# Optimization experiments

Hardware: AMD Instinct MI355X
Metric: run time of the kernel (lower is better)

## Reference

```python
import jax, jax.numpy as jnp
import numpy as np

N = 10000      # nodes
E = 160000     # edges
G = 128        # graphs in batch
DIMS = [16, 32, 32]  # in_channels, then conv output dims
HID = 25       # edge-MLP hidden width
EPS = 1e-5     # batch-norm eps


def setup_inputs() -> dict:
    key = jax.random.key(0)
    ks = iter(jax.random.split(key, 40))
    inp = {}
    inp["x"] = jax.random.normal(next(ks), (N, DIMS[0]), dtype=jnp.float32)
    inp["edge_attr"] = jax.random.uniform(next(ks), (E, 3), dtype=jnp.float32)
    inp["edge_index"] = jax.random.randint(next(ks), (2, E), 0, N, dtype=jnp.int32)
    inp["batch"] = jnp.sort(jax.random.randint(next(ks), (N,), 0, G, dtype=jnp.int32))
    for i in range(2):
        din, dout = DIMS[i], DIMS[i + 1]
        inp[f"w1_{i}"] = jax.random.normal(next(ks), (3, HID), dtype=jnp.float32) * 0.3
        inp[f"b1_{i}"] = jnp.zeros((HID,), jnp.float32)
        inp[f"g_{i}"] = jnp.ones((HID,), jnp.float32)
        inp[f"be_{i}"] = jnp.zeros((HID,), jnp.float32)
        inp[f"w2_{i}"] = jax.random.normal(next(ks), (HID, din * dout), dtype=jnp.float32) * 0.05
        inp[f"b2_{i}"] = jnp.zeros((din * dout,), jnp.float32)
        inp[f"wr_{i}"] = jax.random.normal(next(ks), (din, dout), dtype=jnp.float32) * 0.1
        inp[f"bc_{i}"] = jnp.zeros((dout,), jnp.float32)
    inp["wfc"] = jax.random.normal(next(ks), (DIMS[-1], 1), dtype=jnp.float32) * 0.1
    inp["bfc"] = jnp.zeros((1,), jnp.float32)
    return inp


def _ecn(x, edge_attr, layers, wfc, bfc, edge_index, batch):
    src, dst = edge_index[0], edge_index[1]
    deg = jax.ops.segment_sum(jnp.ones((E,), x.dtype), dst, num_segments=N)
    deg = jnp.clip(deg, 1.0)[:, None]          # [N,1], PyG mean clamps count>=1
    for (w1, b1, g, be, w2, b2, wr, bc) in layers:
        # edge MLP: Linear(3,25) -> BatchNorm(batch stats) -> ReLU -> Linear(25, in*out)
        h = edge_attr @ w1 + b1                 # [E,25]
        mu = h.mean(axis=0)
        var = h.var(axis=0)
        h = (h - mu) * jax.lax.rsqrt(var + EPS) * g + be
        h = jax.nn.relu(h)
        w = (h @ w2 + b2).reshape(E, x.shape[1], -1)   # [E,in,out] per-edge weights
        msg = jnp.einsum('ei,eio->eo', x[src], w)      # gather + per-edge matmul
        agg = jax.ops.segment_sum(msg, dst, num_segments=N) / deg  # scatter-mean
        x = agg + x @ wr + bc                   # root transform + bias
        x = jax.nn.elu(x)
    # global mean pool over graphs
    gsum = jax.ops.segment_sum(x, batch, num_segments=G)
    gcnt = jnp.clip(jax.ops.segment_sum(jnp.ones((N,), x.dtype), batch, num_segments=G), 1.0)
    pooled = gsum / gcnt[:, None]               # [G, dims[-1]]
    return pooled @ wfc + bfc                   # fc MLP last layer is plain Linear


def reference(x, edge_attr, edge_index, batch,
              w1_0, b1_0, g_0, be_0, w2_0, b2_0, wr_0, bc_0,
              w1_1, b1_1, g_1, be_1, w2_1, b2_1, wr_1, bc_1,
              wfc, bfc):
    layers = [
        (w1_0, b1_0, g_0, be_0, w2_0, b2_0, wr_0, bc_0),
        (w1_1, b1_1, g_1, be_1, w2_1, b2_1, wr_1, bc_1),
    ]
    return _ecn(x, edge_attr, layers, wfc, bfc, edge_index, batch)
```

## Files before the change

kernel.cpp:

```cpp
#include <hip/hip_runtime.h>
#include <math.h>

#define NN   10000
#define EE   160000
#define GG   128
#define HIDK 25
#define KROWS 32
#define KB   28
#define DOUT 32
#define EPSBN 1e-5f
#define MOMB 192
#define MAXD 64

#define OFF_CUR   0
#define OFF_GSUM  10016
#define OFF_GMOM  14112
#define OFF_TICK  14128
#define ZERO_FLOATS 14144
#define OFF_W1F0  14144
#define OFF_B1F0  14224
#define OFF_W1F1  14256
#define OFF_B1F1  14336
#define OFF_SRC   14368
#define OFF_EA    654368
#define OFF_WB0   3214368
#define OFF_WB1   3230752
#define OFF_X1    3263520
#define TOTAL_FLOATS 3583520

__device__ inline float wave_red(float v) {
    for (int off = 32; off; off >>= 1) v += __shfl_down(v, off);
    return v;
}

template <int DIN>
__device__ inline void wpack(int idx, const float* __restrict__ w2,
                             const float* __restrict__ b2,
                             const float* __restrict__ wr,
                             const float* __restrict__ bc,
                             float* __restrict__ wbig) {
    int k = idx / (DIN * DOUT);
    int rem = idx - k * (DIN * DOUT);
    int i4 = rem / (4 * DOUT);
    int rem2 = rem - i4 * (4 * DOUT);
    int o = rem2 >> 2, c = rem2 & 3;
    int i = i4 * 4 + c;
    float v = 0.f;
    if (k < HIDK) v = w2[(k * DIN + i) * DOUT + o];
    else if (k == HIDK) v = b2[i * DOUT + o];
    else if (k == HIDK + 1) v = wr[i * DOUT + o];
    else if (k == HIDK + 2) v = (i == 0) ? bc[o] : 0.f;
    wbig[idx] = v;
}

__global__ void k_prep(const float* __restrict__ ea, const int* __restrict__ ei,
                       const float* __restrict__ w2_0, const float* __restrict__ b2_0,
                       const float* __restrict__ wr_0, const float* __restrict__ bc_0,
                       const float* __restrict__ w2_1, const float* __restrict__ b2_1,
                       const float* __restrict__ wr_1, const float* __restrict__ bc_1,
                       const float* __restrict__ w1_0, const float* __restrict__ b1_0,
                       const float* __restrict__ g_0, const float* __restrict__ be_0,
                       const float* __restrict__ w1_1, const float* __restrict__ b1_1,
                       const float* __restrict__ g_1, const float* __restrict__ be_1,
                       float* __restrict__ gmom, int* __restrict__ cur,
                       int* __restrict__ bsrc, float* __restrict__ eab,
                       float* __restrict__ w1f0, float* __restrict__ b1f0,
                       float* __restrict__ w1f1, float* __restrict__ b1f1,
                       float* __restrict__ wb0, float* __restrict__ wb1,
                       int* __restrict__ tick) {
    __shared__ float ls[4][9];
    __shared__ int lastFlag;
    int b = blockIdx.x, t = threadIdx.x;
    int idx = b * 256 + t;

    if (idx < KROWS * 16 * DOUT) wpack<16>(idx, w2_0, b2_0, wr_0, bc_0, wb0);
    else wpack<32>(idx - KROWS * 16 * DOUT, w2_1, b2_1, wr_1, bc_1, wb1);

    float s[9];
#pragma unroll
    for (int j = 0; j < 9; j++) s[j] = 0.f;
    for (int e = idx; e < EE; e += MOMB * 256) {
        float a0 = ea[3 * e], a1 = ea[3 * e + 1], a2 = ea[3 * e + 2];
        s[0] += a0; s[1] += a1; s[2] += a2;
        s[3] += a0 * a0; s[4] += a0 * a1; s[5] += a0 * a2;
        s[6] += a1 * a1; s[7] += a1 * a2; s[8] += a2 * a2;
        int d = ei[EE + e];
        int pos = atomicAdd(cur + d, 1);
        if (pos < MAXD) {
            int slot = d * MAXD + pos;
            bsrc[slot] = ei[e];
            float4 av = { a0, a1, a2, 0.f };
            *(float4*)(eab + 4 * (size_t)slot) = av;
        }
    }
    int w = t >> 6, lane = t & 63;
#pragma unroll
    for (int j = 0; j < 9; j++) {
        float r = wave_red(s[j]);
        if (lane == 0) ls[w][j] = r;
    }
    __syncthreads();
    if (t < 9) atomicAdd(gmom + t, ls[0][t] + ls[1][t] + ls[2][t] + ls[3][t]);

    __threadfence();
    __syncthreads();
    if (t == 0) lastFlag = (atomicAdd(tick, 1) == MOMB - 1);
    __syncthreads();
    if (!lastFlag) return;
    __threadfence();

    if (t < 64) {
        int grp = t >> 5, j = t & 31;
        if (j < HIDK) {
            const float* w1 = grp ? w1_1 : w1_0;
            const float* b1 = grp ? b1_1 : b1_0;
            const float* g  = grp ? g_1  : g_0;
            const float* be = grp ? be_1 : be_0;
            float* w1f = grp ? w1f1 : w1f0;
            float* b1f = grp ? b1f1 : b1f0;
            const float inv = 1.0f / (float)EE;
            float m0 = gmom[0] * inv, m1 = gmom[1] * inv, m2 = gmom[2] * inv;
            float c00 = gmom[3] * inv - m0 * m0, c01 = gmom[4] * inv - m0 * m1;
            float c02 = gmom[5] * inv - m0 * m2, c11 = gmom[6] * inv - m1 * m1;
            float c12 = gmom[7] * inv - m1 * m2, c22 = gmom[8] * inv - m2 * m2;
            float w0 = w1[j], wa = w1[25 + j], wb = w1[50 + j];
            float mean = m0 * w0 + m1 * wa + m2 * wb + b1[j];
            float var = w0 * w0 * c00 + wa * wa * c11 + wb * wb * c22
                      + 2.f * (w0 * wa * c01 + w0 * wb * c02 + wa * wb * c12);
            float sc = g[j] * rsqrtf(var + EPSBN);
            w1f[j] = w0 * sc; w1f[25 + j] = wa * sc; w1f[50 + j] = wb * sc;
            b1f[j] = (b1[j] - mean) * sc + be[j];
        }
    }
}

template <int DIN, int KPL, bool FINAL>
__global__ __launch_bounds__(256, 6)
void k_fused(const int* __restrict__ cnt,
             const int* __restrict__ bsrc,
             const float* __restrict__ eab,
             const float* __restrict__ w1f, const float* __restrict__ b1f,
             const float* __restrict__ wbig, const float* __restrict__ xin,
             const int* __restrict__ batch,
             float* __restrict__ xout, float* __restrict__ gsum) {
    __shared__ __align__(16) float Slds[4][KROWS][DIN];
    __shared__ float Olds[4][4][DOUT];
    __shared__ __align__(16) float hb[4][2][2][32];
    int t = threadIdx.x;
    int w = t >> 6, lane = t & 63;
    int n = blockIdx.x * 4 + w;
    int dg = cnt[n];
    int start = n * MAXD;
    int end = start + (dg > MAXD ? MAXD : dg);

    int il = lane & (DIN - 1);
    int kh = lane / DIN;
    int kme = lane & 31;
    int half = lane >> 5;

    float c0 = 0.f, c1 = 0.f, c2 = 0.f, c3 = 0.f;
    if (kme < HIDK) {
        c0 = w1f[kme]; c1 = w1f[25 + kme]; c2 = w1f[50 + kme]; c3 = b1f[kme];
    } else if (kme == HIDK) {
        c3 = 1.0f;
    }

    float x_own = xin[n * DIN + il];

    float s[KPL];
#pragma unroll
    for (int j = 0; j < KPL; j++) s[j] = 0.f;

    const float4* ea4 = (const float4*)eab;

    int p = start;
    int sA0 = 0, sB0 = 0, vB0 = 0;
    int sA1 = 0, sB1 = 0, vB1 = 0;
    float xA = 0.f, xB = 0.f;
    float4 av1 = {0.f, 0.f, 0.f, 0.f};
    int buf = 0;

    if (p < end) {
        vB0 = (p + 1 < end); int qB0 = vB0 ? p + 1 : p;
        sA0 = bsrc[p]; sB0 = bsrc[qB0];
        int p1 = p + 2;
        if (p1 < end) {
            vB1 = (p1 + 1 < end); int qB1 = vB1 ? p1 + 1 : p1;
            sA1 = bsrc[p1]; sB1 = bsrc[qB1];
            av1 = ea4[half ? qB1 : p1];
        }
        float4 av0 = ea4[half ? qB0 : p];
        xA = xin[sA0 * DIN + il];
        xB = xin[sB0 * DIN + il];
        float hv = av0.x * c0 + av0.y * c1 + av0.z * c2 + c3;
        hv = hv > 0.f ? hv : 0.f;
        hb[w][0][half][kme] = hv;
    }
    while (p < end) {
        int p1 = p + 2, p2 = p + 4;
        int sA2 = 0, sB2 = 0, vB2 = 0;
        float4 av2 = {0.f, 0.f, 0.f, 0.f};
        if (p2 < end) {
            vB2 = (p2 + 1 < end); int qB2 = vB2 ? p2 + 1 : p2;
            sA2 = bsrc[p2]; sB2 = bsrc[qB2];
            av2 = ea4[half ? qB2 : p2];
        }
        float xAn = 0.f, xBn = 0.f;
        if (p1 < end) { xAn = xin[sA1 * DIN + il]; xBn = xin[sB1 * DIN + il]; }
        const float4* hA4 = (const float4*)&hb[w][buf][0][kh * KPL];
        const float4* hB4 = (const float4*)&hb[w][buf][1][kh * KPL];
        float4 ha[KPL / 4], hc[KPL / 4];
#pragma unroll
        for (int j4 = 0; j4 < KPL / 4; j4++) { ha[j4] = hA4[j4]; hc[j4] = hB4[j4]; }
        if (p1 < end) {
            float hv = av1.x * c0 + av1.y * c1 + av1.z * c2 + c3;
            hv = hv > 0.f ? hv : 0.f;
            hb[w][buf ^ 1][half][kme] = hv;
        }
        float xBm = vB0 ? xB : 0.f;
#pragma unroll
        for (int j4 = 0; j4 < KPL / 4; j4++) {
            s[j4 * 4 + 0] += ha[j4].x * xA; s[j4 * 4 + 1] += ha[j4].y * xA;
            s[j4 * 4 + 2] += ha[j4].z * xA; s[j4 * 4 + 3] += ha[j4].w * xA;
        }
#pragma unroll
        for (int j4 = 0; j4 < KPL / 4; j4++) {
            s[j4 * 4 + 0] += hc[j4].x * xBm; s[j4 * 4 + 1] += hc[j4].y * xBm;
            s[j4 * 4 + 2] += hc[j4].z * xBm; s[j4 * 4 + 3] += hc[j4].w * xBm;
        }
        p = p1;
        sA0 = sA1; sB0 = sB1; vB0 = vB1;
        sA1 = sA2; sB1 = sB2; vB1 = vB2;
        xA = xAn; xB = xBn; av1 = av2;
        buf ^= 1;
    }
#pragma unroll
    for (int j = 0; j < KPL; j++)
        Slds[w][kh * KPL + j][il] = s[j];
    float dmul = (float)dg; if (dmul < 1.f) dmul = 1.f;
    if (half == 0) {
        Slds[w][26][il] = dmul * x_own;
        Slds[w][27][il] = (il == 0) ? dmul : 0.f;
    }
    __syncthreads();

    {
        int o = lane & 31, hf = lane >> 5;
        constexpr int I4H = DIN / 8;
        const float4* wb4 = (const float4*)wbig;
        float a0 = 0.f, a1 = 0.f, a2 = 0.f, a3 = 0.f;
        int kbase = w * (KB / 4);
#pragma unroll
        for (int kk = 0; kk < KB / 4; kk++) {
            int k = kbase + kk;
#pragma unroll
            for (int j = 0; j < I4H; j++) {
                int i4 = hf * I4H + j;
                float4 wv = wb4[(k * (DIN / 4) + i4) * 32 + o];
                float4 s0 = *(const float4*)&Slds[0][k][i4 * 4];
                float4 s1 = *(const float4*)&Slds[1][k][i4 * 4];
                float4 s2 = *(const float4*)&Slds[2][k][i4 * 4];
                float4 s3 = *(const float4*)&Slds[3][k][i4 * 4];
                a0 += s0.x * wv.x + s0.y * wv.y + s0.z * wv.z + s0.w * wv.w;
                a1 += s1.x * wv.x + s1.y * wv.y + s1.z * wv.z + s1.w * wv.w;
                a2 += s2.x * wv.x + s2.y * wv.y + s2.z * wv.z + s2.w * wv.w;
                a3 += s3.x * wv.x + s3.y * wv.y + s3.z * wv.z + s3.w * wv.w;
            }
        }
        a0 += __shfl_xor(a0, 32);
        a1 += __shfl_xor(a1, 32);
        a2 += __shfl_xor(a2, 32);
        a3 += __shfl_xor(a3, 32);
        if (hf == 0) {
            Olds[w][0][o] = a0; Olds[w][1][o] = a1;
            Olds[w][2][o] = a2; Olds[w][3][o] = a3;
        }
    }
    __syncthreads();

    if (t < 4 * DOUT) {
        int m = t >> 5, o2 = t & 31;
        int n2 = blockIdx.x * 4 + m;
        float d = (float)cnt[n2]; if (d < 1.f) d = 1.f;
        float r = (Olds[0][m][o2] + Olds[1][m][o2] + Olds[2][m][o2] + Olds[3][m][o2]) / d;
        r = r > 0.f ? r : expm1f(r);
        if (FINAL) atomicAdd(gsum + batch[n2] * DOUT + o2, r);
        else xout[n2 * DOUT + o2] = r;
    }
}

__global__ void k_fc(const float* __restrict__ gsum, const int* __restrict__ batch,
                     const float* __restrict__ wfc, const float* __restrict__ bfc,
                     float* __restrict__ out) {
    int g = threadIdx.x;
    if (g >= GG) return;
    int lo = 0, hi = NN;
    while (lo < hi) { int mid = (lo + hi) >> 1; if (batch[mid] < g) lo = mid + 1; else hi = mid; }
    int lb = lo;
    lo = 0; hi = NN;
    while (lo < hi) { int mid = (lo + hi) >> 1; if (batch[mid] < g + 1) lo = mid + 1; else hi = mid; }
    float c = (float)(lo - lb); if (c < 1.f) c = 1.f;
    float acc = 0.f;
#pragma unroll
    for (int o = 0; o < DOUT; o++) acc += gsum[g * DOUT + o] * wfc[o];
    out[g] = acc / c + bfc[0];
}

extern "C" void kernel_launch(void* const* d_in, const int* in_sizes, int n_in,
                              void* d_out, int out_size, void* d_ws, size_t ws_size,
                              hipStream_t stream) {
    const float* x     = (const float*)d_in[0];
    const float* ea    = (const float*)d_in[1];
    const int*   ei    = (const int*)d_in[2];
    const int*   batch = (const int*)d_in[3];
    const float* w1_0 = (const float*)d_in[4];
    const float* b1_0 = (const float*)d_in[5];
    const float* g_0  = (const float*)d_in[6];
    const float* be_0 = (const float*)d_in[7];
    const float* w2_0 = (const float*)d_in[8];
    const float* b2_0 = (const float*)d_in[9];
    const float* wr_0 = (const float*)d_in[10];
    const float* bc_0 = (const float*)d_in[11];
    const float* w1_1 = (const float*)d_in[12];
    const float* b1_1 = (const float*)d_in[13];
    const float* g_1  = (const float*)d_in[14];
    const float* be_1 = (const float*)d_in[15];
    const float* w2_1 = (const float*)d_in[16];
    const float* b2_1 = (const float*)d_in[17];
    const float* wr_1 = (const float*)d_in[18];
    const float* bc_1 = (const float*)d_in[19];
    const float* wfc  = (const float*)d_in[20];
    const float* bfc  = (const float*)d_in[21];

    float* ws    = (float*)d_ws;
    int*   cur   = (int*)(ws + OFF_CUR);
    float* gsum  = ws + OFF_GSUM;
    float* gmom  = ws + OFF_GMOM;
    int*   tick  = (int*)(ws + OFF_TICK);
    float* w1f0  = ws + OFF_W1F0;
    float* b1f0  = ws + OFF_B1F0;
    float* w1f1  = ws + OFF_W1F1;
    float* b1f1  = ws + OFF_B1F1;
    int*   bsrc  = (int*)(ws + OFF_SRC);
    float* eab   = ws + OFF_EA;
    float* wb0   = ws + OFF_WB0;
    float* wb1   = ws + OFF_WB1;
    float* x1    = ws + OFF_X1;

    hipMemsetAsync(ws, 0, (size_t)ZERO_FLOATS * sizeof(float), stream);

    k_prep<<<MOMB, 256, 0, stream>>>(ea, ei,
                                     w2_0, b2_0, wr_0, bc_0, w2_1, b2_1, wr_1, bc_1,
                                     w1_0, b1_0, g_0, be_0, w1_1, b1_1, g_1, be_1,
                                     gmom, cur, bsrc, eab,
                                     w1f0, b1f0, w1f1, b1f1, wb0, wb1, tick);

    k_fused<16, 8, false><<<NN / 4, 256, 0, stream>>>(cur, bsrc, eab, w1f0, b1f0,
                                                      wb0, x, batch, x1, gsum);
    k_fused<32, 16, true><<<NN / 4, 256, 0, stream>>>(cur, bsrc, eab, w1f1, b1f1,
                                                      wb1, x1, batch, nullptr, gsum);

    k_fc<<<1, 128, 0, stream>>>(gsum, batch, wfc, bfc, (float*)d_out);
}
```

Baseline: 202.8 us.

## Pack source index into edge float4 and widen prep grid to one edge per thread

```diff
diff --git a/kernel.cpp b/kernel.cpp
--- a/kernel.cpp
+++ b/kernel.cpp
@@ -9,24 +9,25 @@
 #define KB   28
 #define DOUT 32
 #define EPSBN 1e-5f
-#define MOMB 192
+#define PREPB 1024
+#define WPACKN (KROWS * 16 * DOUT + KROWS * 32 * DOUT)
 #define MAXD 64
 
 #define OFF_CUR   0
 #define OFF_GSUM  10016
 #define OFF_GMOM  14112
 #define OFF_TICK  14128
-#define ZERO_FLOATS 14144
-#define OFF_W1F0  14144
-#define OFF_B1F0  14224
-#define OFF_W1F1  14256
-#define OFF_B1F1  14336
-#define OFF_SRC   14368
-#define OFF_EA    654368
-#define OFF_WB0   3214368
-#define OFF_WB1   3230752
-#define OFF_X1    3263520
-#define TOTAL_FLOATS 3583520
+#define OFF_GCNT  14144
+#define ZERO_FLOATS 14272
+#define OFF_W1F0  14272
+#define OFF_B1F0  14352
+#define OFF_W1F1  14384
+#define OFF_B1F1  14464
+#define OFF_EA    14496
+#define OFF_WB0   2574496
+#define OFF_WB1   2590880
+#define OFF_X1    2623648
+#define TOTAL_FLOATS 2943648
 
 __device__ inline float wave_red(float v) {
     for (int off = 32; off; off >>= 1) v += __shfl_down(v, off);
@@ -54,6 +55,7 @@
 }
 
 __global__ void k_prep(const float* __restrict__ ea, const int* __restrict__ ei,
+                       const int* __restrict__ batch,
                        const float* __restrict__ w2_0, const float* __restrict__ b2_0,
                        const float* __restrict__ wr_0, const float* __restrict__ bc_0,
                        const float* __restrict__ w2_1, const float* __restrict__ b2_1,
@@ -63,36 +65,37 @@
                        const float* __restrict__ w1_1, const float* __restrict__ b1_1,
                        const float* __restrict__ g_1, const float* __restrict__ be_1,
                        float* __restrict__ gmom, int* __restrict__ cur,
-                       int* __restrict__ bsrc, float* __restrict__ eab,
+                       int* __restrict__ gcnt, float* __restrict__ eab,
                        float* __restrict__ w1f0, float* __restrict__ b1f0,
                        float* __restrict__ w1f1, float* __restrict__ b1f1,
                        float* __restrict__ wb0, float* __restrict__ wb1,
                        int* __restrict__ tick) {
     __shared__ float ls[4][9];
     __shared__ int lastFlag;
-    int b = blockIdx.x, t = threadIdx.x;
-    int idx = b * 256 + t;
+    int t = threadIdx.x;
+    int idx = blockIdx.x * 256 + t;
 
     if (idx < KROWS * 16 * DOUT) wpack<16>(idx, w2_0, b2_0, wr_0, bc_0, wb0);
-    else wpack<32>(idx - KROWS * 16 * DOUT, w2_1, b2_1, wr_1, bc_1, wb1);
+    else if (idx < WPACKN) wpack<32>(idx - KROWS * 16 * DOUT, w2_1, b2_1, wr_1, bc_1, wb1);
 
     float s[9];
 #pragma unroll
     for (int j = 0; j < 9; j++) s[j] = 0.f;
-    for (int e = idx; e < EE; e += MOMB * 256) {
-        float a0 = ea[3 * e], a1 = ea[3 * e + 1], a2 = ea[3 * e + 2];
-        s[0] += a0; s[1] += a1; s[2] += a2;
-        s[3] += a0 * a0; s[4] += a0 * a1; s[5] += a0 * a2;
-        s[6] += a1 * a1; s[7] += a1 * a2; s[8] += a2 * a2;
-        int d = ei[EE + e];
+    if (idx < EE) {
+        float a0 = ea[3 * idx], a1 = ea[3 * idx + 1], a2 = ea[3 * idx + 2];
+        s[0] = a0; s[1] = a1; s[2] = a2;
+        s[3] = a0 * a0; s[4] = a0 * a1; s[5] = a0 * a2;
+        s[6] = a1 * a1; s[7] = a1 * a2; s[8] = a2 * a2;
+        int d = ei[EE + idx];
         int pos = atomicAdd(cur + d, 1);
         if (pos < MAXD) {
             int slot = d * MAXD + pos;
-            bsrc[slot] = ei[e];
-            float4 av = { a0, a1, a2, 0.f };
+            float4 av = { a0, a1, a2, __int_as_float(ei[idx]) };
             *(float4*)(eab + 4 * (size_t)slot) = av;
         }
     }
+    if (idx < NN) atomicAdd(gcnt + batch[idx], 1);
+
     int w = t >> 6, lane = t & 63;
 #pragma unroll
     for (int j = 0; j < 9; j++) {
@@ -100,11 +103,12 @@
         if (lane == 0) ls[w][j] = r;
     }
     __syncthreads();
-    if (t < 9) atomicAdd(gmom + t, ls[0][t] + ls[1][t] + ls[2][t] + ls[3][t]);
+    if (t < 9 && blockIdx.x * 256 < EE)
+        atomicAdd(gmom + t, ls[0][t] + ls[1][t] + ls[2][t] + ls[3][t]);
 
     __threadfence();
     __syncthreads();
-    if (t == 0) lastFlag = (atomicAdd(tick, 1) == MOMB - 1);
+    if (t == 0) lastFlag = (atomicAdd(tick, 1) == PREPB - 1);
     __syncthreads();
     if (!lastFlag) return;
     __threadfence();
@@ -137,7 +141,6 @@
 template <int DIN, int KPL, bool FINAL>
 __global__ __launch_bounds__(256, 6)
 void k_fused(const int* __restrict__ cnt,
-             const int* __restrict__ bsrc,
              const float* __restrict__ eab,
              const float* __restrict__ w1f, const float* __restrict__ b1f,
              const float* __restrict__ wbig, const float* __restrict__ xin,
@@ -174,22 +177,21 @@
     const float4* ea4 = (const float4*)eab;
 
     int p = start;
-    int sA0 = 0, sB0 = 0, vB0 = 0;
-    int sA1 = 0, sB1 = 0, vB1 = 0;
+    int vB0 = 0, vB1 = 0;
     float xA = 0.f, xB = 0.f;
     float4 av1 = {0.f, 0.f, 0.f, 0.f};
     int buf = 0;
 
     if (p < end) {
         vB0 = (p + 1 < end); int qB0 = vB0 ? p + 1 : p;
-        sA0 = bsrc[p]; sB0 = bsrc[qB0];
+        float4 av0 = ea4[half ? qB0 : p];
         int p1 = p + 2;
         if (p1 < end) {
             vB1 = (p1 + 1 < end); int qB1 = vB1 ? p1 + 1 : p1;
-            sA1 = bsrc[p1]; sB1 = bsrc[qB1];
             av1 = ea4[half ? qB1 : p1];
         }
-        float4 av0 = ea4[half ? qB0 : p];
+        int me0 = __float_as_int(av0.w);
+        int sA0 = __shfl(me0, 0), sB0 = __shfl(me0, 32);
         xA = xin[sA0 * DIN + il];
         xB = xin[sB0 * DIN + il];
         float hv = av0.x * c0 + av0.y * c1 + av0.z * c2 + c3;
@@ -198,13 +200,14 @@
     }
     while (p < end) {
         int p1 = p + 2, p2 = p + 4;
-        int sA2 = 0, sB2 = 0, vB2 = 0;
         float4 av2 = {0.f, 0.f, 0.f, 0.f};
+        int vB2 = 0;
         if (p2 < end) {
             vB2 = (p2 + 1 < end); int qB2 = vB2 ? p2 + 1 : p2;
-            sA2 = bsrc[p2]; sB2 = bsrc[qB2];
             av2 = ea4[half ? qB2 : p2];
         }
+        int me1 = __float_as_int(av1.w);
+        int sA1 = __shfl(me1, 0), sB1 = __shfl(me1, 32);
         float xAn = 0.f, xBn = 0.f;
         if (p1 < end) { xAn = xin[sA1 * DIN + il]; xBn = xin[sB1 * DIN + il]; }
         const float4* hA4 = (const float4*)&hb[w][buf][0][kh * KPL];
@@ -229,8 +232,7 @@
             s[j4 * 4 + 2] += hc[j4].z * xBm; s[j4 * 4 + 3] += hc[j4].w * xBm;
         }
         p = p1;
-        sA0 = sA1; sB0 = sB1; vB0 = vB1;
-        sA1 = sA2; sB1 = sB2; vB1 = vB2;
+        vB0 = vB1; vB1 = vB2;
         xA = xAn; xB = xBn; av1 = av2;
         buf ^= 1;
     }
@@ -289,17 +291,12 @@
     }
 }
 
-__global__ void k_fc(const float* __restrict__ gsum, const int* __restrict__ batch,
+__global__ void k_fc(const float* __restrict__ gsum, const int* __restrict__ gcnt,
                      const float* __restrict__ wfc, const float* __restrict__ bfc,
                      float* __restrict__ out) {
     int g = threadIdx.x;
     if (g >= GG) return;
-    int lo = 0, hi = NN;
-    while (lo < hi) { int mid = (lo + hi) >> 1; if (batch[mid] < g) lo = mid + 1; else hi = mid; }
-    int lb = lo;
-    lo = 0; hi = NN;
-    while (lo < hi) { int mid = (lo + hi) >> 1; if (batch[mid] < g + 1) lo = mid + 1; else hi = mid; }
-    float c = (float)(lo - lb); if (c < 1.f) c = 1.f;
+    float c = (float)gcnt[g]; if (c < 1.f) c = 1.f;
     float acc = 0.f;
 #pragma unroll
     for (int o = 0; o < DOUT; o++) acc += gsum[g * DOUT + o] * wfc[o];
@@ -337,11 +334,11 @@
     float* gsum  = ws + OFF_GSUM;
     float* gmom  = ws + OFF_GMOM;
     int*   tick  = (int*)(ws + OFF_TICK);
+    int*   gcnt  = (int*)(ws + OFF_GCNT);
     float* w1f0  = ws + OFF_W1F0;
     float* b1f0  = ws + OFF_B1F0;
     float* w1f1  = ws + OFF_W1F1;
     float* b1f1  = ws + OFF_B1F1;
-    int*   bsrc  = (int*)(ws + OFF_SRC);
     float* eab   = ws + OFF_EA;
     float* wb0   = ws + OFF_WB0;
     float* wb1   = ws + OFF_WB1;
@@ -349,16 +346,16 @@
 
     hipMemsetAsync(ws, 0, (size_t)ZERO_FLOATS * sizeof(float), stream);
 
-    k_prep<<<MOMB, 256, 0, stream>>>(ea, ei,
-                                     w2_0, b2_0, wr_0, bc_0, w2_1, b2_1, wr_1, bc_1,
-                                     w1_0, b1_0, g_0, be_0, w1_1, b1_1, g_1, be_1,
-                                     gmom, cur, bsrc, eab,
-                                     w1f0, b1f0, w1f1, b1f1, wb0, wb1, tick);
-
-    k_fused<16, 8, false><<<NN / 4, 256, 0, stream>>>(cur, bsrc, eab, w1f0, b1f0,
+    k_prep<<<PREPB, 256, 0, stream>>>(ea, ei, batch,
+                                      w2_0, b2_0, wr_0, bc_0, w2_1, b2_1, wr_1, bc_1,
+                                      w1_0, b1_0, g_0, be_0, w1_1, b1_1, g_1, be_1,
+                                      gmom, cur, gcnt, eab,
+                                      w1f0, b1f0, w1f1, b1f1, wb0, wb1, tick);
+
+    k_fused<16, 8, false><<<NN / 4, 256, 0, stream>>>(cur, eab, w1f0, b1f0,
                                                       wb0, x, batch, x1, gsum);
-    k_fused<32, 16, true><<<NN / 4, 256, 0, stream>>>(cur, bsrc, eab, w1f1, b1f1,
+    k_fused<32, 16, true><<<NN / 4, 256, 0, stream>>>(cur, eab, w1f1, b1f1,
                                                       wb1, x1, batch, nullptr, gsum);
 
-    k_fc<<<1, 128, 0, stream>>>(gsum, batch, wfc, bfc, (float*)d_out);
-}
+    k_fc<<<1, 128, 0, stream>>>(gsum, gcnt, wfc, bfc, (float*)d_out);
+}
```

Result: slower. 261.8 us (+29.1%).
